# Kernel tuning notes

Hardware: AMD Instinct MI355X
Metric: run time of the kernel (lower is better)

## Reference

```python
import jax, jax.numpy as jnp
import numpy as np

LN_EPS = 1e-5


def _layernorm_hd(x, gamma, beta):
    # normalize jointly over the last two dims (H, D), matching nn.LayerNorm((H, D))
    m = jnp.mean(x, axis=(-2, -1), keepdims=True)
    v = jnp.var(x, axis=(-2, -1), keepdims=True)
    return (x - m) * jax.lax.rsqrt(v + LN_EPS) * gamma + beta


def setup_inputs() -> dict:
    B, S, H, D = 4, 4096, 8, 64
    key = jax.random.key(0)
    k1, k2, k3 = jax.random.split(key, 3)
    heads_input = jax.random.normal(k1, (B, S, H, D), dtype=jnp.float32)
    W_hid = jax.random.normal(k2, (2 * D, 3 * D), dtype=jnp.float32) * (1.0 / np.sqrt(2 * D))
    b_hid = jnp.zeros((3 * D,), dtype=jnp.float32)
    W_og = jax.random.normal(k3, (2 * D, D), dtype=jnp.float32) * (1.0 / np.sqrt(2 * D))
    b_og = jnp.zeros((D,), dtype=jnp.float32)
    ln_gamma = jnp.ones((H, D), dtype=jnp.float32)
    ln_beta = jnp.zeros((H, D), dtype=jnp.float32)
    init_cx = jnp.zeros((H, D), dtype=jnp.float32)
    return {"heads_input": heads_input, "W_hid": W_hid, "b_hid": b_hid,
            "W_og": W_og, "b_og": b_og, "ln_gamma": ln_gamma,
            "ln_beta": ln_beta, "init_cx": init_cx}


def reference(heads_input, W_hid, b_hid, W_og, b_og, ln_gamma, ln_beta, init_cx):
    B, S, H, D = heads_input.shape
    # RS1cumsumFunc: exclusive (right-shifted) cumsum along seq of detached input
    x_det = jax.lax.stop_gradient(heads_input)
    cs = jnp.cumsum(x_det, axis=1)
    csum_raw = jnp.concatenate([jnp.zeros_like(cs[:, :1]), cs[:, :-1]], axis=1)
    csum = _layernorm_hd(csum_raw, ln_gamma, ln_beta)

    # trans_hid on concat(heads_input, csum): [B,S,H,2D] -> [B,S,H,3D]
    hid_in = jnp.concatenate([heads_input, csum], axis=-1)
    h3 = jnp.einsum('bshd,de->bshe', hid_in, W_hid) + b_hid
    igate, fgate, hidden = jnp.split(h3, 3, axis=-1)
    fg = jax.nn.sigmoid(fgate)
    igh = jax.nn.sigmoid(igate) * jax.nn.relu(hidden)

    # LGateFunc: cell_t = fg_t * cell_{t-1} + igh_t, cell_{-1} = init_cx
    def combine(c1, c2):
        a1, b1 = c1
        a2, b2 = c2
        return a1 * a2, b1 * a2 + b2

    a, b = jax.lax.associative_scan(combine, (fg, igh), axis=1)
    cell = a * init_cx + b  # init_cx [H,D] broadcasts over [B,S,H,D]

    og_in = jnp.concatenate([heads_input, cell], axis=-1)
    og = jax.nn.sigmoid(jnp.einsum('bshd,de->bshe', og_in, W_og) + b_og)
    return og * cell
```

## Files before the change

kernel.cpp:

```cpp
#include <hip/hip_runtime.h>
#include <math.h>

#define S_   4096
#define H_   8
#define D_   64
#define HD_  512
#define NCH  256
#define LCH  16
#define RC   128

typedef __bf16 bf16x8 __attribute__((ext_vector_type(8)));
typedef float  f32x4  __attribute__((ext_vector_type(4)));

__device__ __forceinline__ float sigm(float v) { return 1.f / (1.f + __expf(-v)); }

__global__ __launch_bounds__(256) void k_wt(const float* __restrict__ Wh,
                                            const float* __restrict__ Wo,
                                            __bf16* __restrict__ Wth,
                                            __bf16* __restrict__ Wto) {
  int idx = blockIdx.x * 256 + threadIdx.x;
  if (idx < 24576) {
    int k = idx / 192, n = idx % 192;
    Wth[n * 128 + k] = (__bf16)Wh[idx];
  } else {
    int j = idx - 24576;
    int k = j >> 6, n = j & 63;
    Wto[n * 128 + k] = (__bf16)Wo[j];
  }
}

__global__ __launch_bounds__(512) void k_chunk_sums(const float* __restrict__ x,
                                                    float* __restrict__ sums) {
  const int b = blockIdx.x >> 8, c = blockIdx.x & 255;
  const int t = threadIdx.x;
  const float* p = x + ((size_t)b * S_ + c * LCH) * HD_ + t;
  float acc = 0.f;
  #pragma unroll
  for (int i = 0; i < LCH; ++i) acc += p[(size_t)i * HD_];
  sums[((size_t)b * NCH + c) * HD_ + t] = acc;
}

__global__ __launch_bounds__(512) void k_scan_offsets(float* __restrict__ sums) {
  const int b = blockIdx.x, t = threadIdx.x;
  float run = 0.f;
  for (int c = 0; c < NCH; ++c) {
    size_t idx = ((size_t)b * NCH + c) * HD_ + t;
    float v = sums[idx];
    sums[idx] = run;
    run += v;
  }
}

__global__ __launch_bounds__(512) void k_ln(const float* __restrict__ x,
                                            const float* __restrict__ offs,
                                            const float* __restrict__ gamma,
                                            const float* __restrict__ beta,
                                            __bf16* __restrict__ Abf) {
  __shared__ float2 red[2][8];
  const int b = blockIdx.x >> 8, c = blockIdx.x & 255;
  const int t = threadIdx.x;
  float run = offs[((size_t)b * NCH + c) * HD_ + t];
  const float g = gamma[t], be = beta[t];
  const size_t xbase = ((size_t)b * S_ + c * LCH) * HD_ + t;
  const int h = t >> 6, d = t & 63;
  float xv = x[xbase];
  for (int i = 0; i < LCH; ++i) {
    float xn = (i < LCH - 1) ? x[xbase + (size_t)(i + 1) * HD_] : 0.f;
    float v = run, v2 = run * run;
    #pragma unroll
    for (int o = 32; o; o >>= 1) { v += __shfl_xor(v, o); v2 += __shfl_xor(v2, o); }
    if ((t & 63) == 0) red[i & 1][t >> 6] = make_float2(v, v2);
    __syncthreads();
    float s1 = 0.f, s2 = 0.f;
    #pragma unroll
    for (int w = 0; w < 8; ++w) { s1 += red[i & 1][w].x; s2 += red[i & 1][w].y; }
    float m = s1 * (1.f / HD_);
    float var = fmaf(-m, m, s2 * (1.f / HD_));
    float inv = rsqrtf(var + 1e-5f);
    size_t r = ((size_t)b * S_ + c * LCH + i) * H_ + h;
    Abf[r * 128 + 64 + d] = (__bf16)((run - m) * inv * g + be);
    Abf[r * 128 + d] = (__bf16)xv;
    run += xv;
    xv = xn;
  }
}

__global__ __launch_bounds__(256) void k_gates(const __bf16* __restrict__ Abf,
                                               const __bf16* __restrict__ Wt,
                                               const float* __restrict__ bh,
                                               float* __restrict__ fg,
                                               float* __restrict__ igh,
                                               float* __restrict__ cA,
                                               float* __restrict__ cB) {
  __shared__ float fgl[RC * 68];
  __shared__ float ighl[RC * 68];
  const int t = threadIdx.x;
  const int wave = t >> 6, lane = t & 63;
  const int quad = lane >> 4, l16 = lane & 15;
  const int r0 = blockIdx.x * RC;

  f32x4 acc[2][12];
  #pragma unroll
  for (int i = 0; i < 2; ++i)
    #pragma unroll
    for (int j = 0; j < 12; ++j) acc[i][j] = (f32x4){0.f, 0.f, 0.f, 0.f};

  #pragma unroll
  for (int ks = 0; ks < 4; ++ks) {
    bf16x8 bfrag[12];
    #pragma unroll
    for (int nt = 0; nt < 12; ++nt)
      bfrag[nt] = *(const bf16x8*)(Wt + (nt * 16 + l16) * 128 + ks * 32 + quad * 8);
    #pragma unroll
    for (int mi = 0; mi < 2; ++mi) {
      int mt = wave * 2 + mi;
      bf16x8 afrag = *(const bf16x8*)(Abf + (size_t)(r0 + mt * 16 + l16) * 128 + ks * 32 + quad * 8);
      #pragma unroll
      for (int nt = 0; nt < 12; ++nt)
        acc[mi][nt] = __builtin_amdgcn_mfma_f32_16x16x32_bf16(afrag, bfrag[nt], acc[mi][nt], 0, 0, 0);
    }
  }

  #pragma unroll
  for (int mi = 0; mi < 2; ++mi) {
    int mt = wave * 2 + mi;
    #pragma unroll
    for (int nt = 0; nt < 4; ++nt) {
      int d = nt * 16 + l16;
      float bi = bh[d], bf = bh[64 + d], bhv = bh[128 + d];
      #pragma unroll
      for (int r = 0; r < 4; ++r) {
        int row = mt * 16 + quad * 4 + r;
        float ip = acc[mi][nt][r] + bi;
        float fp = acc[mi][nt + 4][r] + bf;
        float hp = acc[mi][nt + 8][r] + bhv;
        fgl[row * 68 + d] = sigm(fp);
        ighl[row * 68 + d] = sigm(ip) * fmaxf(hp, 0.f);
      }
    }
  }
  __syncthreads();

  #pragma unroll
  for (int rep = 0; rep < 8; ++rep) {
    int idx = rep * 256 + t;
    int row = idx >> 4, c4 = idx & 15;
    float4 vf = *(const float4*)&fgl[row * 68 + c4 * 4];
    float4 vg = *(const float4*)&ighl[row * 68 + c4 * 4];
    ((float4*)fg)[(size_t)(r0 + row) * 16 + c4] = vf;
    ((float4*)igh)[(size_t)(r0 + row) * 16 + c4] = vg;
  }

  #pragma unroll
  for (int p = 0; p < 2; ++p) {
    int hd = p * 256 + t;
    int h = hd >> 6, d = hd & 63;
    float a = 1.f, bb = 0.f;
    #pragma unroll
    for (int s = 0; s < LCH; ++s) {
      float f = fgl[(s * 8 + h) * 68 + d];
      float g = ighl[(s * 8 + h) * 68 + d];
      a *= f;
      bb = fmaf(bb, f, g);
    }
    cA[(size_t)blockIdx.x * 512 + hd] = a;
    cB[(size_t)blockIdx.x * 512 + hd] = bb;
  }
}

__global__ __launch_bounds__(512) void k_cell_scan(float* __restrict__ cA,
                                                   const float* __restrict__ cB,
                                                   const float* __restrict__ initcx) {
  const int b = blockIdx.x, t = threadIdx.x;
  float run = initcx[t];
  for (int c = 0; c < NCH; ++c) {
    size_t idx = ((size_t)b * NCH + c) * HD_ + t;
    float a = cA[idx], bb = cB[idx];
    cA[idx] = run;
    run = fmaf(a, run, bb);
  }
}

__global__ __launch_bounds__(256) void k_og(const __bf16* __restrict__ Abf,
                                            const float* __restrict__ fg,
                                            const float* __restrict__ igh,
                                            const float* __restrict__ cin,
                                            const __bf16* __restrict__ Wt,
                                            const float* __restrict__ bo,
                                            float* __restrict__ out) {
  __shared__ float cl[RC * 68];
  const int t = threadIdx.x;
  const int wave = t >> 6, lane = t & 63;
  const int quad = lane >> 4, l16 = lane & 15;
  const int r0 = blockIdx.x * RC;

  #pragma unroll
  for (int p = 0; p < 2; ++p) {
    int hd = p * 256 + t;
    int h = hd >> 6, d = hd & 63;
    float run = cin[(size_t)blockIdx.x * 512 + hd];
    #pragma unroll
    for (int s = 0; s < LCH; ++s) {
      size_t row = (size_t)r0 + s * 8 + h;
      run = fmaf(fg[row * 64 + d], run, igh[row * 64 + d]);
      cl[(s * 8 + h) * 68 + d] = run;
    }
  }
  __syncthreads();

  f32x4 acc[2][4];
  #pragma unroll
  for (int i = 0; i < 2; ++i)
    #pragma unroll
    for (int j = 0; j < 4; ++j) acc[i][j] = (f32x4){0.f, 0.f, 0.f, 0.f};

  #pragma unroll
  for (int ks = 0; ks < 4; ++ks) {
    bf16x8 bfrag[4];
    #pragma unroll
    for (int nt = 0; nt < 4; ++nt)
      bfrag[nt] = *(const bf16x8*)(Wt + (nt * 16 + l16) * 128 + ks * 32 + quad * 8);
    #pragma unroll
    for (int mi = 0; mi < 2; ++mi) {
      int mt = wave * 2 + mi;
      bf16x8 afrag;
      if (ks < 2) {
        afrag = *(const bf16x8*)(Abf + (size_t)(r0 + mt * 16 + l16) * 128 + ks * 32 + quad * 8);
      } else {
        int rowl = mt * 16 + l16;
        const float* src = &cl[rowl * 68 + (ks - 2) * 32 + quad * 8];
        #pragma unroll
        for (int j = 0; j < 8; ++j) afrag[j] = (__bf16)src[j];
      }
      #pragma unroll
      for (int nt = 0; nt < 4; ++nt)
        acc[mi][nt] = __builtin_amdgcn_mfma_f32_16x16x32_bf16(afrag, bfrag[nt], acc[mi][nt], 0, 0, 0);
    }
  }

  #pragma unroll
  for (int mi = 0; mi < 2; ++mi) {
    int mt = wave * 2 + mi;
    #pragma unroll
    for (int nt = 0; nt < 4; ++nt) {
      int d = nt * 16 + l16;
      float bv = bo[d];
      #pragma unroll
      for (int r = 0; r < 4; ++r) {
        int rowl = mt * 16 + quad * 4 + r;
        float og = sigm(acc[mi][nt][r] + bv);
        out[(size_t)(r0 + rowl) * 64 + d] = og * cl[rowl * 68 + d];
      }
    }
  }
}

extern "C" void kernel_launch(void* const* d_in, const int* in_sizes, int n_in,
                              void* d_out, int out_size, void* d_ws, size_t ws_size,
                              hipStream_t stream) {
  const float* x      = (const float*)d_in[0];
  const float* W_hid  = (const float*)d_in[1];
  const float* b_hid  = (const float*)d_in[2];
  const float* W_og   = (const float*)d_in[3];
  const float* b_og   = (const float*)d_in[4];
  const float* gamma  = (const float*)d_in[5];
  const float* beta   = (const float*)d_in[6];
  const float* initcx = (const float*)d_in[7];
  float* out = (float*)d_out;
  float* ws  = (float*)d_ws;

  float*  buf0 = ws;
  float*  buf1 = ws + 524288;
  __bf16* Abf  = (__bf16*)(ws + 1048576);
  float*  fgv  = ws + 1048576 + 8388608;
  float*  ighv = fgv + 8388608;
  __bf16* Wth  = (__bf16*)(ighv + 8388608);
  __bf16* Wto  = Wth + 24576;

  k_wt         <<<128,  256, 0, stream>>>(W_hid, W_og, Wth, Wto);
  k_chunk_sums <<<1024, 512, 0, stream>>>(x, buf0);
  k_scan_offsets<<<4,   512, 0, stream>>>(buf0);
  k_ln         <<<1024, 512, 0, stream>>>(x, buf0, gamma, beta, Abf);
  k_gates      <<<1024, 256, 0, stream>>>(Abf, Wth, b_hid, fgv, ighv, buf0, buf1);
  k_cell_scan  <<<4,    512, 0, stream>>>(buf0, buf1, initcx);
  k_og         <<<1024, 256, 0, stream>>>(Abf, fgv, ighv, buf0, Wto, b_og, out);
}
```

Before: 221.1 us.

## Reorder rows head-major so in-chunk cell scan runs in MFMA registers

Intermediate rows within each chunk are now stored head-major, so every 16-row MFMA tile holds one head across the 16 sequence steps. The gates kernel can then do the local forget/input scan directly on accumulator registers, using cross-quad shuffles instead of staging through shared memory. It writes the prefix coefficients (A, B), so the output kernel only needs one fma per element rather than a serial 16-step loop. The two serial scan kernels are also batched into groups of 8 loads to expose memory-level parallelism. The output store is remapped back to the original layout, which makes those writes less contiguous.

```diff
diff --git a/kernel.cpp b/kernel.cpp
--- a/kernel.cpp
+++ b/kernel.cpp
@@ -43,11 +43,16 @@
 __global__ __launch_bounds__(512) void k_scan_offsets(float* __restrict__ sums) {
   const int b = blockIdx.x, t = threadIdx.x;
   float run = 0.f;
-  for (int c = 0; c < NCH; ++c) {
-    size_t idx = ((size_t)b * NCH + c) * HD_ + t;
-    float v = sums[idx];
-    sums[idx] = run;
-    run += v;
+  for (int c0 = 0; c0 < NCH; c0 += 8) {
+    float v[8];
+    #pragma unroll
+    for (int i = 0; i < 8; ++i)
+      v[i] = sums[((size_t)b * NCH + c0 + i) * HD_ + t];
+    #pragma unroll
+    for (int i = 0; i < 8; ++i) {
+      sums[((size_t)b * NCH + c0 + i) * HD_ + t] = run;
+      run += v[i];
+    }
   }
 }
 
@@ -63,6 +68,7 @@
   const float g = gamma[t], be = beta[t];
   const size_t xbase = ((size_t)b * S_ + c * LCH) * HD_ + t;
   const int h = t >> 6, d = t & 63;
+  const size_t rbase = ((size_t)b * NCH + c) * 128 + h * 16;
   float xv = x[xbase];
   for (int i = 0; i < LCH; ++i) {
     float xn = (i < LCH - 1) ? x[xbase + (size_t)(i + 1) * HD_] : 0.f;
@@ -77,7 +83,7 @@
     float m = s1 * (1.f / HD_);
     float var = fmaf(-m, m, s2 * (1.f / HD_));
     float inv = rsqrtf(var + 1e-5f);
-    size_t r = ((size_t)b * S_ + c * LCH + i) * H_ + h;
+    size_t r = rbase + i;
     Abf[r * 128 + 64 + d] = (__bf16)((run - m) * inv * g + be);
     Abf[r * 128 + d] = (__bf16)xv;
     run += xv;
@@ -88,12 +94,10 @@
 __global__ __launch_bounds__(256) void k_gates(const __bf16* __restrict__ Abf,
                                                const __bf16* __restrict__ Wt,
                                                const float* __restrict__ bh,
-                                               float* __restrict__ fg,
-                                               float* __restrict__ igh,
+                                               float* __restrict__ ga,
+                                               float* __restrict__ gb,
                                                float* __restrict__ cA,
                                                float* __restrict__ cB) {
-  __shared__ float fgl[RC * 68];
-  __shared__ float ighl[RC * 68];
   const int t = threadIdx.x;
   const int wave = t >> 6, lane = t & 63;
   const int quad = lane >> 4, l16 = lane & 15;
@@ -126,45 +130,43 @@
     int mt = wave * 2 + mi;
     #pragma unroll
     for (int nt = 0; nt < 4; ++nt) {
-      int d = nt * 16 + l16;
-      float bi = bh[d], bf = bh[64 + d], bhv = bh[128 + d];
+      int dcol = nt * 16 + l16;
+      float bi = bh[dcol], bf_ = bh[64 + dcol], bhv = bh[128 + dcol];
+      float pa[4], pb[4];
+      float a = 1.f, bb = 0.f;
       #pragma unroll
       for (int r = 0; r < 4; ++r) {
-        int row = mt * 16 + quad * 4 + r;
         float ip = acc[mi][nt][r] + bi;
-        float fp = acc[mi][nt + 4][r] + bf;
+        float fp = acc[mi][nt + 4][r] + bf_;
         float hp = acc[mi][nt + 8][r] + bhv;
-        fgl[row * 68 + d] = sigm(fp);
-        ighl[row * 68 + d] = sigm(ip) * fmaxf(hp, 0.f);
-      }
-    }
-  }
-  __syncthreads();
-
-  #pragma unroll
-  for (int rep = 0; rep < 8; ++rep) {
-    int idx = rep * 256 + t;
-    int row = idx >> 4, c4 = idx & 15;
-    float4 vf = *(const float4*)&fgl[row * 68 + c4 * 4];
-    float4 vg = *(const float4*)&ighl[row * 68 + c4 * 4];
-    ((float4*)fg)[(size_t)(r0 + row) * 16 + c4] = vf;
-    ((float4*)igh)[(size_t)(r0 + row) * 16 + c4] = vg;
-  }
-
-  #pragma unroll
-  for (int p = 0; p < 2; ++p) {
-    int hd = p * 256 + t;
-    int h = hd >> 6, d = hd & 63;
-    float a = 1.f, bb = 0.f;
-    #pragma unroll
-    for (int s = 0; s < LCH; ++s) {
-      float f = fgl[(s * 8 + h) * 68 + d];
-      float g = ighl[(s * 8 + h) * 68 + d];
-      a *= f;
-      bb = fmaf(bb, f, g);
-    }
-    cA[(size_t)blockIdx.x * 512 + hd] = a;
-    cB[(size_t)blockIdx.x * 512 + hd] = bb;
+        float fv = sigm(fp);
+        float gv = sigm(ip) * fmaxf(hp, 0.f);
+        a = fv * a;
+        bb = fmaf(fv, bb, gv);
+        pa[r] = a; pb[r] = bb;
+      }
+      float exA = 1.f, exB = 0.f;
+      #pragma unroll
+      for (int q = 0; q < 3; ++q) {
+        float Aq = __shfl(a, q * 16 + l16, 64);
+        float Bq = __shfl(bb, q * 16 + l16, 64);
+        if (q < quad) { exB = fmaf(Aq, exB, Bq); exA = Aq * exA; }
+      }
+      float ra3 = 0.f, rb3 = 0.f;
+      #pragma unroll
+      for (int r = 0; r < 4; ++r) {
+        float ra = pa[r] * exA;
+        float rb = fmaf(pa[r], exB, pb[r]);
+        size_t row = (size_t)(r0 + mt * 16 + quad * 4 + r);
+        ga[row * 64 + dcol] = ra;
+        gb[row * 64 + dcol] = rb;
+        ra3 = ra; rb3 = rb;
+      }
+      if (quad == 3) {
+        cA[(size_t)blockIdx.x * 512 + mt * 64 + dcol] = ra3;
+        cB[(size_t)blockIdx.x * 512 + mt * 64 + dcol] = rb3;
+      }
+    }
   }
 }
 
@@ -173,17 +175,26 @@
                                                    const float* __restrict__ initcx) {
   const int b = blockIdx.x, t = threadIdx.x;
   float run = initcx[t];
-  for (int c = 0; c < NCH; ++c) {
-    size_t idx = ((size_t)b * NCH + c) * HD_ + t;
-    float a = cA[idx], bb = cB[idx];
-    cA[idx] = run;
-    run = fmaf(a, run, bb);
+  for (int c0 = 0; c0 < NCH; c0 += 8) {
+    float av[8], bv[8];
+    #pragma unroll
+    for (int i = 0; i < 8; ++i) {
+      size_t idx = ((size_t)b * NCH + c0 + i) * HD_ + t;
+      av[i] = cA[idx];
+      bv[i] = cB[idx];
+    }
+    #pragma unroll
+    for (int i = 0; i < 8; ++i) {
+      size_t idx = ((size_t)b * NCH + c0 + i) * HD_ + t;
+      cA[idx] = run;
+      run = fmaf(av[i], run, bv[i]);
+    }
   }
 }
 
 __global__ __launch_bounds__(256) void k_og(const __bf16* __restrict__ Abf,
-                                            const float* __restrict__ fg,
-                                            const float* __restrict__ igh,
+                                            const float* __restrict__ ga,
+                                            const float* __restrict__ gb,
                                             const float* __restrict__ cin,
                                             const __bf16* __restrict__ Wt,
                                             const float* __restrict__ bo,
@@ -193,17 +204,22 @@
   const int wave = t >> 6, lane = t & 63;
   const int quad = lane >> 4, l16 = lane & 15;
   const int r0 = blockIdx.x * RC;
-
-  #pragma unroll
-  for (int p = 0; p < 2; ++p) {
-    int hd = p * 256 + t;
-    int h = hd >> 6, d = hd & 63;
-    float run = cin[(size_t)blockIdx.x * 512 + hd];
-    #pragma unroll
-    for (int s = 0; s < LCH; ++s) {
-      size_t row = (size_t)r0 + s * 8 + h;
-      run = fmaf(fg[row * 64 + d], run, igh[row * 64 + d]);
-      cl[(s * 8 + h) * 68 + d] = run;
+  const int b4 = blockIdx.x >> 8, c = blockIdx.x & 255;
+
+  #pragma unroll
+  for (int mi = 0; mi < 2; ++mi) {
+    int mt = wave * 2 + mi;
+    #pragma unroll
+    for (int nt = 0; nt < 4; ++nt) {
+      int dcol = nt * 16 + l16;
+      float ci = cin[(size_t)blockIdx.x * 512 + mt * 64 + dcol];
+      #pragma unroll
+      for (int r = 0; r < 4; ++r) {
+        int rowl = mt * 16 + quad * 4 + r;
+        size_t row = (size_t)(r0 + rowl);
+        float cv = fmaf(ga[row * 64 + dcol], ci, gb[row * 64 + dcol]);
+        cl[rowl * 68 + dcol] = cv;
+      }
     }
   }
   __syncthreads();
@@ -243,13 +259,14 @@
     int mt = wave * 2 + mi;
     #pragma unroll
     for (int nt = 0; nt < 4; ++nt) {
-      int d = nt * 16 + l16;
-      float bv = bo[d];
+      int dcol = nt * 16 + l16;
+      float bv = bo[dcol];
       #pragma unroll
       for (int r = 0; r < 4; ++r) {
         int rowl = mt * 16 + quad * 4 + r;
+        int s = quad * 4 + r;
         float og = sigm(acc[mi][nt][r] + bv);
-        out[(size_t)(r0 + rowl) * 64 + d] = og * cl[rowl * 68 + d];
+        out[(((size_t)b4 * S_ + c * LCH + s) * H_ + mt) * 64 + dcol] = og * cl[rowl * 68 + dcol];
       }
     }
   }
@@ -272,16 +289,16 @@
   float*  buf0 = ws;
   float*  buf1 = ws + 524288;
   __bf16* Abf  = (__bf16*)(ws + 1048576);
-  float*  fgv  = ws + 1048576 + 8388608;
-  float*  ighv = fgv + 8388608;
-  __bf16* Wth  = (__bf16*)(ighv + 8388608);
+  float*  ga   = ws + 1048576 + 8388608;
+  float*  gb   = ga + 8388608;
+  __bf16* Wth  = (__bf16*)(gb + 8388608);
   __bf16* Wto  = Wth + 24576;
 
-  k_wt         <<<128,  256, 0, stream>>>(W_hid, W_og, Wth, Wto);
-  k_chunk_sums <<<1024, 512, 0, stream>>>(x, buf0);
-  k_scan_offsets<<<4,   512, 0, stream>>>(buf0);
-  k_ln         <<<1024, 512, 0, stream>>>(x, buf0, gamma, beta, Abf);
-  k_gates      <<<1024, 256, 0, stream>>>(Abf, Wth, b_hid, fgv, ighv, buf0, buf1);
-  k_cell_scan  <<<4,    512, 0, stream>>>(buf0, buf1, initcx);
-  k_og         <<<1024, 256, 0, stream>>>(Abf, fgv, ighv, buf0, Wto, b_og, out);
-}
+  k_wt          <<<128,  256, 0, stream>>>(W_hid, W_og, Wth, Wto);
+  k_chunk_sums  <<<1024, 512, 0, stream>>>(x, buf0);
+  k_scan_offsets<<<4,    512, 0, stream>>>(buf0);
+  k_ln          <<<1024, 512, 0, stream>>>(x, buf0, gamma, beta, Abf);
+  k_gates       <<<1024, 256, 0, stream>>>(Abf, Wth, b_hid, ga, gb, buf0, buf1);
+  k_cell_scan   <<<4,    512, 0, stream>>>(buf0, buf1, initcx);
+  k_og          <<<1024, 256, 0, stream>>>(Abf, ga, gb, buf0, Wto, b_og, out);
+}
```

Result: no change. 223.1 us (+0.9%).
